# Kernel optimization log

Measured on AMD Instinct MI355X. Metric: run time of the kernel, lower is better.

## Reference

```python
import jax, jax.numpy as jnp
import numpy as np


def setup_inputs() -> dict:
    key = jax.random.key(0)
    ks = jax.random.split(key, 7)
    D, N = 32, 3            # directions, ambient dim
    K0, K1, K2 = 500_000, 1_500_000, 1_000_000  # verts, edges, tris
    H = 256                 # num_heights
    return {
        "dirs": jax.random.normal(ks[0], (D, N), jnp.float32),
        "v_coords": jax.random.normal(ks[1], (K0, N), jnp.float32),
        "v_weights": jax.random.uniform(ks[2], (K0,), jnp.float32),
        "edge_verts": jax.random.randint(ks[3], (K1, 2), 0, K0),
        "edge_weights": jax.random.uniform(ks[4], (K1,), jnp.float32),
        "tri_verts": jax.random.randint(ks[5], (K2, 3), 0, K0),
        "tri_weights": jax.random.uniform(ks[6], (K2,), jnp.float32),
        "num_heights": H,
    }


def reference(dirs, v_coords, v_weights, edge_verts, edge_weights,
              tri_verts, tri_weights, num_heights):
    eps = 1e-12
    h = int(num_heights)
    d = dirs.shape[0]
    # L2-normalize directions (torch F.normalize with eps clamp on the norm)
    dirs = dirs / jnp.maximum(jnp.linalg.norm(dirs, axis=1, keepdims=True), eps)

    # vertex height indices: (K0, d)
    v_norms = jnp.linalg.norm(v_coords, axis=1)
    max_height = jnp.maximum(jnp.max(v_norms), eps)
    v_heights = v_coords @ dirs.T
    v_indices = jnp.clip(
        jnp.ceil((h - 1) * (max_height + v_heights) / (2.0 * max_height)),
        0, h - 1,
    ).astype(jnp.int32)

    dir_idx = jnp.arange(d)[None, :]  # broadcast against (k_i, d) bin indices
    diff_wect = jnp.zeros((d, h), jnp.float32)
    # 0-simplices (vertices), sign +1
    diff_wect = diff_wect.at[dir_idx, v_indices].add(v_weights[:, None])
    # 1-simplices (edges), sign (-1)^1 = -1: gather + max over the 2 verts
    edge_bins = jnp.max(v_indices[edge_verts], axis=1)   # (K1, d)
    diff_wect = diff_wect.at[dir_idx, edge_bins].add(-edge_weights[:, None])
    # 2-simplices (triangles), sign (+1): gather + max over the 3 verts
    tri_bins = jnp.max(v_indices[tri_verts], axis=1)     # (K2, d)
    diff_wect = diff_wect.at[dir_idx, tri_bins].add(tri_weights[:, None])

    return jnp.cumsum(diff_wect, axis=1)  # (d, h)
```

## Files before the change

kernel.cpp:

```cpp
#include <hip/hip_runtime.h>
#include <math.h>

#define NDIR 32
#define NH   256
#define BLK  512
#define NB   1024
#define PACKB 256
#define UNIT 128
#define SCALE    2048.0f
#define INVSCALE (1.0 / 2048.0)
#define BIAS  128.5f

#define CV 64
#define CE 96
#define CT 128

#define WS_DIRS 8
#define WS_BMAX 128
#define WS_TAB  512

typedef _Float16 half2v __attribute__((ext_vector_type(2)));

__device__ __forceinline__ unsigned rfl_u(unsigned x) { return __builtin_amdgcn_readfirstlane(x); }

__device__ __forceinline__ unsigned pack2(float x, float y) {
    union { half2v h; unsigned u; } c;
    c.h = half2v{(_Float16)x, (_Float16)y};
    return c.u;
}
__device__ __forceinline__ half2v upk(unsigned u) {
    union { unsigned u; half2v h; } c; c.u = u; return c.h;
}
__device__ __forceinline__ float hdot(half2v a, half2v b, float acc) {
#if __has_builtin(__builtin_amdgcn_fdot2)
    return __builtin_amdgcn_fdot2(a, b, acc, false);
#else
    return acc + (float)a.x * (float)b.x + (float)a.y * (float)b.y;
#endif
}
__device__ __forceinline__ int bin_of(float hs) {
    return (int)fminf(fmaxf(hs, 0.0f), 255.0f);
}

template <bool PACKED>
__global__ void __launch_bounds__(512) wect_prep_kernel(
    const float* __restrict__ dirs, const float* __restrict__ vc, int K0,
    int P, int part_off, float* __restrict__ ws)
{
    int tid  = blockIdx.x * blockDim.x + threadIdx.x;
    int nthr = gridDim.x * blockDim.x;
    for (int i = tid; i < P * NDIR * NH; i += nthr)
        ((int*)ws)[part_off + i] = 0;
    if (blockIdx.x == 0 && threadIdx.x >= 64 && threadIdx.x < 64 + NDIR) {
        int d = threadIdx.x - 64;
        float x = dirs[d * 3 + 0], y = dirs[d * 3 + 1], z = dirs[d * 3 + 2];
        float n = fmaxf(sqrtf(x * x + y * y + z * z), 1e-12f);
        ws[WS_DIRS + d * 3 + 0] = x / n;
        ws[WS_DIRS + d * 3 + 1] = y / n;
        ws[WS_DIRS + d * 3 + 2] = z / n;
    }
    float m = 0.0f;
    uint2* tab = (uint2*)(ws + WS_TAB);
    for (int i = tid; i < K0; i += nthr) {
        float x = vc[3 * i + 0], y = vc[3 * i + 1], z = vc[3 * i + 2];
        m = fmaxf(m, x * x + y * y + z * z);
        if (PACKED) tab[i] = make_uint2(pack2(x, y), pack2(z, 0.0f));
    }
    __shared__ float wm[8];
    #pragma unroll
    for (int off = 32; off > 0; off >>= 1)
        m = fmaxf(m, __shfl_down(m, off, 64));
    if ((threadIdx.x & 63) == 0) wm[threadIdx.x >> 6] = m;
    __syncthreads();
    if (threadIdx.x == 0) {
        float r = wm[0];
        #pragma unroll
        for (int i = 1; i < 8; ++i) r = fmaxf(r, wm[i]);
        ws[WS_BMAX + blockIdx.x] = r;
    }
}

__device__ __forceinline__ int cost_to_unit(long long cost, int N0, int N1,
                                            long long C0, long long C1) {
    if (cost <= C0) return (int)((cost + (CV - 1)) / CV);
    cost -= C0;
    if (cost <= C1) return N0 + (int)((cost + (CE - 1)) / CE);
    cost -= C1;
    return N0 + N1 + (int)((cost + (CT - 1)) / CT);
}

template <bool PACKED>
__global__ void __launch_bounds__(BLK, 8) wect_hist_kernel(
    const float* __restrict__ vc, const float* __restrict__ vw,
    const int*   __restrict__ ev, const float* __restrict__ ew,
    const int*   __restrict__ tv, const float* __restrict__ tw,
    int K0, int K1, int K2, int N0, int N1, int N2,
    long long C0, long long C1, long long Ctot,
    int P, int part_off, float* __restrict__ ws)
{
    __shared__ int hist[NDIR * NH];
    for (int i = threadIdx.x; i < NDIR * NH; i += BLK) hist[i] = 0;

    const int wave = threadIdx.x >> 6;
    const int lane = threadIdx.x & 63;

    float m = 0.0f;
    for (int i = lane; i < PACKB; i += 64) m = fmaxf(m, ws[WS_BMAX + i]);
    #pragma unroll
    for (int off = 32; off > 0; off >>= 1)
        m = fmaxf(m, __shfl_xor(m, off, 64));
    float maxh = fmaxf(sqrtf(m), 1e-12f);
    float inv  = 127.5f / maxh;

    unsigned sdxy[NDIR], sdz[NDIR];
    #pragma unroll
    for (int d = 0; d < NDIR; ++d) {
        float dx = ws[WS_DIRS + 3 * d + 0] * inv;
        float dy = ws[WS_DIRS + 3 * d + 1] * inv;
        float dz = ws[WS_DIRS + 3 * d + 2] * inv;
        sdxy[d] = rfl_u(pack2(dx, dy));
        sdz[d]  = rfl_u(pack2(dz, 0.0f));
    }
    __syncthreads();

    const uint2* tab = (const uint2*)(ws + WS_TAB);
    #define LDC(J, CXY, CZ)                                                  \
        do {                                                                 \
            if constexpr (PACKED) {                                          \
                uint2 r = tab[J];                                            \
                CXY = upk(r.x); CZ = upk(r.y);                               \
            } else {                                                         \
                float _x = vc[3 * (J) + 0], _y = vc[3 * (J) + 1], _z = vc[3 * (J) + 2]; \
                CXY = half2v{(_Float16)_x, (_Float16)_y};                    \
                CZ  = half2v{(_Float16)_z, (_Float16)0.0f};                  \
            }                                                                \
        } while (0)

    const int W = NB * 8;
    long long gw = (long long)blockIdx.x * 8 + wave;
    int u0 = cost_to_unit(gw * Ctot / W, N0, N1, C0, C1);
    int u1 = cost_to_unit((gw + 1) * Ctot / W, N0, N1, C0, C1);

    for (int u = u0; u < u1; ++u) {
        if (u < N0) {
            int base = u * UNIT;
            half2v xy[2], z[2]; int w[2];
            #pragma unroll
            for (int k = 0; k < 2; ++k) {
                int i = base + k * 64 + lane;
                int j = (i < K0) ? i : 0;
                LDC(j, xy[k], z[k]);
                w[k] = (i < K0) ? __float2int_rn(vw[j] * SCALE) : 0;
            }
            #pragma unroll
            for (int d = 0; d < NDIR; ++d) {
                half2v dxy = upk(sdxy[d]), dz = upk(sdz[d]);
                #pragma unroll
                for (int k = 0; k < 2; ++k) {
                    float h = hdot(xy[k], dxy, hdot(z[k], dz, BIAS));
                    atomicAdd(&hist[d * NH + bin_of(h)], w[k]);
                }
            }
        } else if (u < N0 + N1) {
            int base = (u - N0) * UNIT;
            half2v axy[2], az[2], bxy[2], bz[2]; int w[2];
            #pragma unroll
            for (int k = 0; k < 2; ++k) {
                int i = base + k * 64 + lane;
                int j = (i < K1) ? i : 0;
                int2 e = ((const int2*)ev)[j];
                LDC(e.x, axy[k], az[k]);
                LDC(e.y, bxy[k], bz[k]);
                w[k] = (i < K1) ? -__float2int_rn(ew[j] * SCALE) : 0;
            }
            #pragma unroll
            for (int d = 0; d < NDIR; ++d) {
                half2v dxy = upk(sdxy[d]), dz = upk(sdz[d]);
                #pragma unroll
                for (int k = 0; k < 2; ++k) {
                    float h = fmaxf(hdot(axy[k], dxy, hdot(az[k], dz, BIAS)),
                                    hdot(bxy[k], dxy, hdot(bz[k], dz, BIAS)));
                    atomicAdd(&hist[d * NH + bin_of(h)], w[k]);
                }
            }
        } else {
            int base = (u - N0 - N1) * UNIT;
            half2v axy[2], az[2], bxy[2], bz[2], cxy[2], cz[2]; int w[2];
            #pragma unroll
            for (int k = 0; k < 2; ++k) {
                int i = base + k * 64 + lane;
                int j = (i < K2) ? i : 0;
                int va = tv[3 * j + 0], vb = tv[3 * j + 1], vcc = tv[3 * j + 2];
                LDC(va,  axy[k], az[k]);
                LDC(vb,  bxy[k], bz[k]);
                LDC(vcc, cxy[k], cz[k]);
                w[k] = (i < K2) ? __float2int_rn(tw[j] * SCALE) : 0;
            }
            #pragma unroll
            for (int d = 0; d < NDIR; ++d) {
                half2v dxy = upk(sdxy[d]), dz = upk(sdz[d]);
                #pragma unroll
                for (int k = 0; k < 2; ++k) {
                    float h = fmaxf(fmaxf(hdot(axy[k], dxy, hdot(az[k], dz, BIAS)),
                                          hdot(bxy[k], dxy, hdot(bz[k], dz, BIAS))),
                                    hdot(cxy[k], dxy, hdot(cz[k], dz, BIAS)));
                    atomicAdd(&hist[d * NH + bin_of(h)], w[k]);
                }
            }
        }
    }
    #undef LDC

    __syncthreads();
    int* part = (int*)ws + part_off + (blockIdx.x & (P - 1)) * (NDIR * NH);
    for (int i = threadIdx.x; i < NDIR * NH; i += BLK) {
        int v = hist[i];
        if (v != 0) atomicAdd(&part[i], v);
    }
}

__global__ void wect_reduce_kernel(const float* __restrict__ ws, int P, int part_off,
                                   float* __restrict__ out) {
    __shared__ long long s[NH];
    int d = blockIdx.x, h = threadIdx.x;
    const int* part = (const int*)ws + part_off + d * NH + h;
    long long acc = 0;
    #pragma unroll 4
    for (int p = 0; p < P; ++p)
        acc += (long long)part[p * (NDIR * NH)];
    s[h] = acc;
    __syncthreads();
    #pragma unroll
    for (int off = 1; off < NH; off <<= 1) {
        long long v = (h >= off) ? s[h - off] : 0;
        __syncthreads();
        s[h] += v;
        __syncthreads();
    }
    out[d * NH + h] = (float)((double)s[h] * INVSCALE);
}

extern "C" void kernel_launch(void* const* d_in, const int* in_sizes, int n_in,
                              void* d_out, int out_size, void* d_ws, size_t ws_size,
                              hipStream_t stream) {
    const float* dirs = (const float*)d_in[0];
    const float* vc   = (const float*)d_in[1];
    const float* vw   = (const float*)d_in[2];
    const int*   ev   = (const int*)d_in[3];
    const float* ew   = (const float*)d_in[4];
    const int*   tv   = (const int*)d_in[5];
    const float* tw   = (const float*)d_in[6];
    int K0 = in_sizes[2];
    int K1 = in_sizes[4];
    int K2 = in_sizes[6];

    float* ws  = (float*)d_ws;
    float* out = (float*)d_out;

    long long words = (long long)(ws_size / 4);

    int  part_off = WS_TAB + 2 * K0;
    bool packed   = (words - part_off) >= 8LL * NDIR * NH;
    if (!packed) part_off = WS_TAB;

    long long availP = (words - part_off) / (NDIR * NH);
    int P = 1;
    while (P * 2 <= availP && P < 64) P *= 2;

    int N0 = (K0 + UNIT - 1) / UNIT;
    int N1 = (K1 + UNIT - 1) / UNIT;
    int N2 = (K2 + UNIT - 1) / UNIT;
    long long C0 = (long long)N0 * CV;
    long long C1 = (long long)N1 * CE;
    long long Ctot = C0 + C1 + (long long)N2 * CT;

    if (packed) {
        wect_prep_kernel<true><<<PACKB, 512, 0, stream>>>(dirs, vc, K0, P, part_off, ws);
        wect_hist_kernel<true><<<NB, BLK, 0, stream>>>(
            vc, vw, ev, ew, tv, tw, K0, K1, K2, N0, N1, N2, C0, C1, Ctot, P, part_off, ws);
    } else {
        wect_prep_kernel<false><<<PACKB, 512, 0, stream>>>(dirs, vc, K0, P, part_off, ws);
        wect_hist_kernel<false><<<NB, BLK, 0, stream>>>(
            vc, vw, ev, ew, tv, tw, K0, K1, K2, N0, N1, N2, C0, C1, Ctot, P, part_off, ws);
    }
    wect_reduce_kernel<<<NDIR, NH, 0, stream>>>(ws, P, part_off, out);
}
```

Measured before the change: 70.57 us.

## Replace static per-wave cost partition with sharded atomic work-stealing counters

Work units are no longer split statically across waves by cost. Each block is mapped to one of eight shards. Each wave starts on a fixed unit inside its shard and then pulls further units from a per-shard global atomic counter, which the prep kernel initializes. The aim is to even out load imbalance from variable gather latency and late-starting blocks. In exchange it adds a global atomic per unit, which is padded to separate cache lines, and it makes the order in which units are processed non-deterministic.

```diff
diff --git a/kernel.cpp b/kernel.cpp
--- a/kernel.cpp
+++ b/kernel.cpp
@@ -7,6 +7,8 @@
 #define NB   1024
 #define PACKB 256
 #define UNIT 128
+#define NSHARD 8
+#define WPS  ((NB * 8) / NSHARD)
 #define SCALE    2048.0f
 #define INVSCALE (1.0 / 2048.0)
 #define BIAS  128.5f
@@ -17,6 +19,7 @@
 
 #define WS_DIRS 8
 #define WS_BMAX 128
+#define WS_CTR  384
 #define WS_TAB  512
 
 typedef _Float16 half2v __attribute__((ext_vector_type(2)));
@@ -42,15 +45,30 @@
     return (int)fminf(fmaxf(hs, 0.0f), 255.0f);
 }
 
+__device__ __forceinline__ int cost_to_unit(long long cost, int N0, int N1,
+                                            long long C0, long long C1) {
+    if (cost <= C0) return (int)((cost + (CV - 1)) / CV);
+    cost -= C0;
+    if (cost <= C1) return N0 + (int)((cost + (CE - 1)) / CE);
+    cost -= C1;
+    return N0 + N1 + (int)((cost + (CT - 1)) / CT);
+}
+
 template <bool PACKED>
 __global__ void __launch_bounds__(512) wect_prep_kernel(
     const float* __restrict__ dirs, const float* __restrict__ vc, int K0,
+    int N0, int N1, long long C0, long long C1, long long Ctot,
     int P, int part_off, float* __restrict__ ws)
 {
     int tid  = blockIdx.x * blockDim.x + threadIdx.x;
     int nthr = gridDim.x * blockDim.x;
     for (int i = tid; i < P * NDIR * NH; i += nthr)
         ((int*)ws)[part_off + i] = 0;
+    if (blockIdx.x == 0 && threadIdx.x < NSHARD) {
+        long long cs = (long long)threadIdx.x * Ctot / NSHARD;
+        ((int*)ws)[WS_CTR + threadIdx.x * 16] =
+            cost_to_unit(cs, N0, N1, C0, C1) + WPS;
+    }
     if (blockIdx.x == 0 && threadIdx.x >= 64 && threadIdx.x < 64 + NDIR) {
         int d = threadIdx.x - 64;
         float x = dirs[d * 3 + 0], y = dirs[d * 3 + 1], z = dirs[d * 3 + 2];
@@ -78,15 +96,6 @@
         for (int i = 1; i < 8; ++i) r = fmaxf(r, wm[i]);
         ws[WS_BMAX + blockIdx.x] = r;
     }
-}
-
-__device__ __forceinline__ int cost_to_unit(long long cost, int N0, int N1,
-                                            long long C0, long long C1) {
-    if (cost <= C0) return (int)((cost + (CV - 1)) / CV);
-    cost -= C0;
-    if (cost <= C1) return N0 + (int)((cost + (CE - 1)) / CE);
-    cost -= C1;
-    return N0 + N1 + (int)((cost + (CT - 1)) / CT);
 }
 
 template <bool PACKED>
@@ -136,12 +145,17 @@
             }                                                                \
         } while (0)
 
-    const int W = NB * 8;
-    long long gw = (long long)blockIdx.x * 8 + wave;
-    int u0 = cost_to_unit(gw * Ctot / W, N0, N1, C0, C1);
-    int u1 = cost_to_unit((gw + 1) * Ctot / W, N0, N1, C0, C1);
-
-    for (int u = u0; u < u1; ++u) {
+    const int shard = blockIdx.x & (NSHARD - 1);
+    const int Us = cost_to_unit((long long)shard * Ctot / NSHARD, N0, N1, C0, C1);
+    const int Ue = cost_to_unit((long long)(shard + 1) * Ctot / NSHARD, N0, N1, C0, C1);
+    int* ctr = (int*)ws + WS_CTR + shard * 16;
+    int cur = Us + ((blockIdx.x >> 3) << 3) + wave;
+
+    while (cur < Ue) {
+        int nxt = 0;
+        if (lane == 0) nxt = atomicAdd(ctr, 1);
+        const int u = cur;
+
         if (u < N0) {
             int base = u * UNIT;
             half2v xy[2], z[2]; int w[2];
@@ -208,6 +222,8 @@
                 }
             }
         }
+
+        cur = __shfl(nxt, 0, 64);
     }
     #undef LDC
 
@@ -275,11 +291,13 @@
     long long Ctot = C0 + C1 + (long long)N2 * CT;
 
     if (packed) {
-        wect_prep_kernel<true><<<PACKB, 512, 0, stream>>>(dirs, vc, K0, P, part_off, ws);
+        wect_prep_kernel<true><<<PACKB, 512, 0, stream>>>(
+            dirs, vc, K0, N0, N1, C0, C1, Ctot, P, part_off, ws);
         wect_hist_kernel<true><<<NB, BLK, 0, stream>>>(
             vc, vw, ev, ew, tv, tw, K0, K1, K2, N0, N1, N2, C0, C1, Ctot, P, part_off, ws);
     } else {
-        wect_prep_kernel<false><<<PACKB, 512, 0, stream>>>(dirs, vc, K0, P, part_off, ws);
+        wect_prep_kernel<false><<<PACKB, 512, 0, stream>>>(
+            dirs, vc, K0, N0, N1, C0, C1, Ctot, P, part_off, ws);
         wect_hist_kernel<false><<<NB, BLK, 0, stream>>>(
             vc, vw, ev, ew, tv, tw, K0, K1, K2, N0, N1, N2, C0, C1, Ctot, P, part_off, ws);
     }
```

Result: slower. 115.0 us (+62.9%).

## Replace static cost-partitioned work split with per-block dynamic wave work counter

Applied to the files above, without the earlier changes.

Work is now split into 64-element units, assigned round-robin across blocks (unit = block + n*NB), and each wave claims its next unit from a per-block shared-memory atomic counter instead of a static cost-model range. This balances load between waves with different simplex types and removes the hand-tuned cost constants. It also caps the number of partial histograms at 16 and zeroes shared memory with int4 stores. The price is one LDS atomic plus a shuffle per unit, and less memory-level parallelism per iteration because each lane now loads one element per unit instead of two.

```diff
diff --git a/kernel.cpp b/kernel.cpp
--- a/kernel.cpp
+++ b/kernel.cpp
@@ -6,14 +6,10 @@
 #define BLK  512
 #define NB   1024
 #define PACKB 256
-#define UNIT 128
+#define UNIT 64
 #define SCALE    2048.0f
 #define INVSCALE (1.0 / 2048.0)
 #define BIAS  128.5f
-
-#define CV 64
-#define CE 96
-#define CT 128
 
 #define WS_DIRS 8
 #define WS_BMAX 128
@@ -80,29 +76,24 @@
     }
 }
 
-__device__ __forceinline__ int cost_to_unit(long long cost, int N0, int N1,
-                                            long long C0, long long C1) {
-    if (cost <= C0) return (int)((cost + (CV - 1)) / CV);
-    cost -= C0;
-    if (cost <= C1) return N0 + (int)((cost + (CE - 1)) / CE);
-    cost -= C1;
-    return N0 + N1 + (int)((cost + (CT - 1)) / CT);
-}
-
 template <bool PACKED>
 __global__ void __launch_bounds__(BLK, 8) wect_hist_kernel(
     const float* __restrict__ vc, const float* __restrict__ vw,
     const int*   __restrict__ ev, const float* __restrict__ ew,
     const int*   __restrict__ tv, const float* __restrict__ tw,
-    int K0, int K1, int K2, int N0, int N1, int N2,
-    long long C0, long long C1, long long Ctot,
+    int K0, int K1, int K2, int N0, int N01, int Ntot,
     int P, int part_off, float* __restrict__ ws)
 {
     __shared__ int hist[NDIR * NH];
-    for (int i = threadIdx.x; i < NDIR * NH; i += BLK) hist[i] = 0;
+    __shared__ int nctr;
+    for (int i = threadIdx.x; i < (NDIR * NH) / 4; i += BLK)
+        ((int4*)hist)[i] = make_int4(0, 0, 0, 0);
 
     const int wave = threadIdx.x >> 6;
     const int lane = threadIdx.x & 63;
+    const int b    = blockIdx.x;
+    const int nu   = (Ntot - b + NB - 1) / NB;
+    if (threadIdx.x == 0) nctr = 8;
 
     float m = 0.0f;
     for (int i = lane; i < PACKB; i += 64) m = fmaxf(m, ws[WS_BMAX + i]);
@@ -136,78 +127,59 @@
             }                                                                \
         } while (0)
 
-    const int W = NB * 8;
-    long long gw = (long long)blockIdx.x * 8 + wave;
-    int u0 = cost_to_unit(gw * Ctot / W, N0, N1, C0, C1);
-    int u1 = cost_to_unit((gw + 1) * Ctot / W, N0, N1, C0, C1);
-
-    for (int u = u0; u < u1; ++u) {
+    int n = wave;
+    while (n < nu) {
+        int nxt = 0;
+        if (lane == 0) nxt = atomicAdd(&nctr, 1);
+        const int u = b + n * NB;
+
         if (u < N0) {
-            int base = u * UNIT;
-            half2v xy[2], z[2]; int w[2];
-            #pragma unroll
-            for (int k = 0; k < 2; ++k) {
-                int i = base + k * 64 + lane;
-                int j = (i < K0) ? i : 0;
-                LDC(j, xy[k], z[k]);
-                w[k] = (i < K0) ? __float2int_rn(vw[j] * SCALE) : 0;
-            }
+            int i = u * UNIT + lane;
+            int j = (i < K0) ? i : 0;
+            half2v xy, z;
+            LDC(j, xy, z);
+            int w = (i < K0) ? __float2int_rn(vw[j] * SCALE) : 0;
             #pragma unroll
             for (int d = 0; d < NDIR; ++d) {
                 half2v dxy = upk(sdxy[d]), dz = upk(sdz[d]);
-                #pragma unroll
-                for (int k = 0; k < 2; ++k) {
-                    float h = hdot(xy[k], dxy, hdot(z[k], dz, BIAS));
-                    atomicAdd(&hist[d * NH + bin_of(h)], w[k]);
-                }
+                float h = hdot(xy, dxy, hdot(z, dz, BIAS));
+                atomicAdd(&hist[d * NH + bin_of(h)], w);
             }
-        } else if (u < N0 + N1) {
-            int base = (u - N0) * UNIT;
-            half2v axy[2], az[2], bxy[2], bz[2]; int w[2];
-            #pragma unroll
-            for (int k = 0; k < 2; ++k) {
-                int i = base + k * 64 + lane;
-                int j = (i < K1) ? i : 0;
-                int2 e = ((const int2*)ev)[j];
-                LDC(e.x, axy[k], az[k]);
-                LDC(e.y, bxy[k], bz[k]);
-                w[k] = (i < K1) ? -__float2int_rn(ew[j] * SCALE) : 0;
-            }
+        } else if (u < N01) {
+            int i = (u - N0) * UNIT + lane;
+            int j = (i < K1) ? i : 0;
+            int2 e = ((const int2*)ev)[j];
+            half2v axy, az, bxy, bz;
+            LDC(e.x, axy, az);
+            LDC(e.y, bxy, bz);
+            int w = (i < K1) ? -__float2int_rn(ew[j] * SCALE) : 0;
             #pragma unroll
             for (int d = 0; d < NDIR; ++d) {
                 half2v dxy = upk(sdxy[d]), dz = upk(sdz[d]);
-                #pragma unroll
-                for (int k = 0; k < 2; ++k) {
-                    float h = fmaxf(hdot(axy[k], dxy, hdot(az[k], dz, BIAS)),
-                                    hdot(bxy[k], dxy, hdot(bz[k], dz, BIAS)));
-                    atomicAdd(&hist[d * NH + bin_of(h)], w[k]);
-                }
+                float h = fmaxf(hdot(axy, dxy, hdot(az, dz, BIAS)),
+                                hdot(bxy, dxy, hdot(bz, dz, BIAS)));
+                atomicAdd(&hist[d * NH + bin_of(h)], w);
             }
         } else {
-            int base = (u - N0 - N1) * UNIT;
-            half2v axy[2], az[2], bxy[2], bz[2], cxy[2], cz[2]; int w[2];
-            #pragma unroll
-            for (int k = 0; k < 2; ++k) {
-                int i = base + k * 64 + lane;
-                int j = (i < K2) ? i : 0;
-                int va = tv[3 * j + 0], vb = tv[3 * j + 1], vcc = tv[3 * j + 2];
-                LDC(va,  axy[k], az[k]);
-                LDC(vb,  bxy[k], bz[k]);
-                LDC(vcc, cxy[k], cz[k]);
-                w[k] = (i < K2) ? __float2int_rn(tw[j] * SCALE) : 0;
-            }
+            int i = (u - N01) * UNIT + lane;
+            int j = (i < K2) ? i : 0;
+            int va = tv[3 * j + 0], vb = tv[3 * j + 1], vcc = tv[3 * j + 2];
+            half2v axy, az, bxy, bz, cxy, cz;
+            LDC(va,  axy, az);
+            LDC(vb,  bxy, bz);
+            LDC(vcc, cxy, cz);
+            int w = (i < K2) ? __float2int_rn(tw[j] * SCALE) : 0;
             #pragma unroll
             for (int d = 0; d < NDIR; ++d) {
                 half2v dxy = upk(sdxy[d]), dz = upk(sdz[d]);
-                #pragma unroll
-                for (int k = 0; k < 2; ++k) {
-                    float h = fmaxf(fmaxf(hdot(axy[k], dxy, hdot(az[k], dz, BIAS)),
-                                          hdot(bxy[k], dxy, hdot(bz[k], dz, BIAS))),
-                                    hdot(cxy[k], dxy, hdot(cz[k], dz, BIAS)));
-                    atomicAdd(&hist[d * NH + bin_of(h)], w[k]);
-                }
+                float h = fmaxf(fmaxf(hdot(axy, dxy, hdot(az, dz, BIAS)),
+                                      hdot(bxy, dxy, hdot(bz, dz, BIAS))),
+                                hdot(cxy, dxy, hdot(cz, dz, BIAS)));
+                atomicAdd(&hist[d * NH + bin_of(h)], w);
             }
         }
+
+        n = __shfl(nxt, 0, 64);
     }
     #undef LDC
 
@@ -265,23 +237,22 @@
 
     long long availP = (words - part_off) / (NDIR * NH);
     int P = 1;
-    while (P * 2 <= availP && P < 64) P *= 2;
+    while (P * 2 <= availP && P < 16) P *= 2;
 
     int N0 = (K0 + UNIT - 1) / UNIT;
     int N1 = (K1 + UNIT - 1) / UNIT;
     int N2 = (K2 + UNIT - 1) / UNIT;
-    long long C0 = (long long)N0 * CV;
-    long long C1 = (long long)N1 * CE;
-    long long Ctot = C0 + C1 + (long long)N2 * CT;
+    int N01 = N0 + N1;
+    int Ntot = N01 + N2;
 
     if (packed) {
         wect_prep_kernel<true><<<PACKB, 512, 0, stream>>>(dirs, vc, K0, P, part_off, ws);
         wect_hist_kernel<true><<<NB, BLK, 0, stream>>>(
-            vc, vw, ev, ew, tv, tw, K0, K1, K2, N0, N1, N2, C0, C1, Ctot, P, part_off, ws);
+            vc, vw, ev, ew, tv, tw, K0, K1, K2, N0, N01, Ntot, P, part_off, ws);
     } else {
         wect_prep_kernel<false><<<PACKB, 512, 0, stream>>>(dirs, vc, K0, P, part_off, ws);
         wect_hist_kernel<false><<<NB, BLK, 0, stream>>>(
-            vc, vw, ev, ew, tv, tw, K0, K1, K2, N0, N1, N2, C0, C1, Ctot, P, part_off, ws);
+            vc, vw, ev, ew, tv, tw, K0, K1, K2, N0, N01, Ntot, P, part_off, ws);
     }
     wect_reduce_kernel<<<NDIR, NH, 0, stream>>>(ws, P, part_off, out);
 }
```

After: 62.10 us. 12.0% less time.
